# Kernel tuning notes

Measured on AMD Instinct MI355X. Metric: run time of the kernel, lower is better.

The kernel has to match this reference:

```python
import jax, jax.numpy as jnp
import numpy as np

NUM_GROUPS = 8
NUM_HEADS = 4
EPS = 1e-5


def group_norm(x, w, b):
    # x: [B, C, H, W]; normalize over (C/G, H, W) within each of G groups
    B, C, H, W = x.shape
    xg = x.reshape(B, NUM_GROUPS, C // NUM_GROUPS, H, W)
    mean = xg.mean(axis=(2, 3, 4), keepdims=True)
    var = xg.var(axis=(2, 3, 4), keepdims=True)
    xn = ((xg - mean) * jax.lax.rsqrt(var + EPS)).reshape(B, C, H, W)
    return xn * w[None, :, None, None] + b[None, :, None, None]


def setup_inputs() -> dict:
    key = jax.random.key(0)
    ks = jax.random.split(key, 7)
    B, C, H, W = 4, 256, 64, 64
    x = jax.random.normal(ks[0], (B, C, H, W), dtype=jnp.float32)
    gn_w = jax.random.normal(ks[1], (C,), dtype=jnp.float32) * 0.1 + 1.0
    gn_b = jax.random.normal(ks[2], (C,), dtype=jnp.float32) * 0.1
    qkv_w = jax.random.normal(ks[3], (3 * C, C), dtype=jnp.float32) / np.sqrt(C)
    qkv_b = jax.random.normal(ks[4], (3 * C,), dtype=jnp.float32) * 0.02
    proj_w = jax.random.normal(ks[5], (C, C), dtype=jnp.float32) / np.sqrt(C)
    proj_b = jax.random.normal(ks[6], (C,), dtype=jnp.float32) * 0.02
    return {"x": x, "gn_w": gn_w, "gn_b": gn_b, "qkv_w": qkv_w,
            "qkv_b": qkv_b, "proj_w": proj_w, "proj_b": proj_b}


def reference(x, gn_w, gn_b, qkv_w, qkv_b, proj_w, proj_b):
    B, C, H, W = x.shape
    nh = NUM_HEADS
    hd = C // nh
    scale = hd ** -0.5
    N = H * W

    h = group_norm(x, gn_w, gn_b)
    # 1x1 conv == channel matmul: [B, 3C, H, W]
    qkv = jnp.einsum('oc,bchw->bohw', qkv_w, h) + qkv_b[None, :, None, None]
    qkv = qkv.reshape(B, 3, nh, hd, N)  # matches torch .view(B,3,nh,hd,HW)
    q, k, v = qkv[:, 0], qkv[:, 1], qkv[:, 2]  # each [B, nh, hd, N]

    attn = jnp.einsum('bhdn,bhdm->bhnm', q, k) * scale  # [B, nh, N, N]
    attn = jax.nn.softmax(attn, axis=-1)
    out = jnp.einsum('bhnm,bhdm->bhdn', attn, v)  # [B, nh, hd, N]
    out = out.reshape(B, C, H, W)

    proj = jnp.einsum('oc,bchw->bohw', proj_w, out) + proj_b[None, :, None, None]
    return x + proj
```

## Files before the change

kernel.cpp:

```cpp
#include <hip/hip_runtime.h>
#include <hip/hip_bf16.h>

#define BB   4
#define CC   256
#define NN   4096
#define NH   4
#define HD   64
#define NG   8
#define GSZ  32
#define EPSV 1e-5f
#define SCALE_L2E 0.18033688f

typedef __bf16 bf16x8 __attribute__((ext_vector_type(8)));
typedef float  f32x4  __attribute__((ext_vector_type(4)));
typedef short  short4v __attribute__((ext_vector_type(4)));

#define MFMA16(a, b, c)  __builtin_amdgcn_mfma_f32_16x16x32_bf16((a), (b), (c), 0, 0, 0)
#define MFMAPV(a, b, c)  __builtin_amdgcn_mfma_f32_16x16x16bf16_1k((a), (b), (c), 0, 0, 0)

#if __has_builtin(__builtin_amdgcn_exp2f)
#define EXP2F __builtin_amdgcn_exp2f
#else
#define EXP2F exp2f
#endif

__device__ inline unsigned short f2bf(float f) {
    unsigned int u = __float_as_uint(f);
    u += 0x7fffu + ((u >> 16) & 1u);
    return (unsigned short)(u >> 16);
}

__device__ __forceinline__ short4v pk4(const f32x4& p) {
    alignas(8) unsigned int u[2];
    u[0] = __builtin_amdgcn_perm(__float_as_uint(p[1]), __float_as_uint(p[0]), 0x07060302u);
    u[1] = __builtin_amdgcn_perm(__float_as_uint(p[3]), __float_as_uint(p[2]), 0x07060302u);
    return *reinterpret_cast<short4v*>(u);
}

__device__ __forceinline__ void async_ld16(void* lds, const void* g) {
    __builtin_amdgcn_global_load_lds(
        (const __attribute__((address_space(1))) unsigned int*)g,
        (__attribute__((address_space(3))) unsigned int*)lds, 16, 0, 0);
}

__global__ void k_prep(const float* __restrict__ x, float* __restrict__ stats,
                       const float* __restrict__ wq, const float* __restrict__ wp,
                       unsigned short* __restrict__ oq, unsigned short* __restrict__ op) {
    int blk = blockIdx.x;
    int t = threadIdx.x;
    if (blk >= 256) {
        int i = (blk - 256) * 256 + t;
        if (i < 3 * CC * CC) oq[i] = f2bf(wq[i]);
        if (i < CC * CC)     op[i] = f2bf(wp[i]);
        return;
    }
    int b = blk >> 6, g = (blk >> 3) & 7, s = blk & 7;
    const float* p = x + ((size_t)(b * CC + g * GSZ)) * NN + s * 16384;
    float s0 = 0.f, s1 = 0.f;
    #pragma unroll
    for (int i = 0; i < 64; ++i) { float v = p[i * 256 + t]; s0 += v; s1 += v * v; }
    #pragma unroll
    for (int m = 1; m <= 32; m <<= 1) { s0 += __shfl_xor(s0, m); s1 += __shfl_xor(s1, m); }
    __shared__ float ls[8];
    int w = t >> 6;
    if ((t & 63) == 0) { ls[w * 2] = s0; ls[w * 2 + 1] = s1; }
    __syncthreads();
    if (t == 0) {
        float a0 = ls[0] + ls[2] + ls[4] + ls[6];
        float a1 = ls[1] + ls[3] + ls[5] + ls[7];
        atomicAdd(&stats[(b * NG + g) * 2 + 0], a0);
        atomicAdd(&stats[(b * NG + g) * 2 + 1], a1);
    }
}

__global__ void k_gnapply(const float* __restrict__ x, const float* __restrict__ gw,
                          const float* __restrict__ gb, const float* __restrict__ stats,
                          unsigned short* __restrict__ ht) {
    int b = blockIdx.z, ct = blockIdx.y, nt = blockIdx.x;
    int c0 = ct * 32, n0 = nt * 64;
    int t = threadIdx.x;
    __shared__ float tile[32][65];
    const float* xp = x + ((size_t)(b * CC + c0)) * NN + n0;
    int cl = t >> 6, nl = t & 63;
    #pragma unroll
    for (int p = 0; p < 8; ++p)
        tile[p * 4 + cl][nl] = xp[(size_t)(p * 4 + cl) * NN + nl];
    float sum = stats[(b * NG + ct) * 2 + 0];
    float ssq = stats[(b * NG + ct) * 2 + 1];
    float mean = sum * (1.0f / 131072.0f);
    float var  = ssq * (1.0f / 131072.0f) - mean * mean;
    float inv  = rsqrtf(var + EPSV);
    __syncthreads();
    int nw = t >> 2, ci = (t & 3) * 8;
    alignas(16) unsigned short o8[8];
    #pragma unroll
    for (int j = 0; j < 8; ++j) {
        int c = c0 + ci + j;
        float v = (tile[ci + j][nw] - mean) * inv * gw[c] + gb[c];
        o8[j] = f2bf(v);
    }
    *reinterpret_cast<uint4*>(ht + ((size_t)(b * NN + n0 + nw)) * CC + c0 + ci) =
        *reinterpret_cast<const uint4*>(o8);
}

__global__ void __launch_bounds__(256)
k_qkv(const unsigned short* __restrict__ ht, const unsigned short* __restrict__ wq,
      const float* __restrict__ qb,
      unsigned short* __restrict__ qt, unsigned short* __restrict__ kt,
      unsigned short* __restrict__ vt) {
    int bx = blockIdx.x, by = blockIdx.y;
    int t = threadIdx.x, wave = t >> 6, lane = t & 63;
    int l15 = lane & 15, quad = lane >> 4;
    int wm = wave >> 1, wn = wave & 1;

    __shared__ alignas(16) unsigned char At[2][8192];
    __shared__ alignas(16) unsigned char Bt[2][8192];

    const char* Ag = (const char*)wq + (size_t)by * 65536;
    const char* Bg = (const char*)ht + (size_t)bx * 65536;
    int row0 = t >> 2, slot = t & 3;
    size_t a0 = (size_t)row0 * 512 + slot * 16;
    size_t a1 = a0 + 64 * 512;
    unsigned int dst0 = wave * 1024;

    auto stage = [&](int buf, int kk) {
        size_t ko = (size_t)kk * 64;
        async_ld16(At[buf] + dst0,        Ag + a0 + ko);
        async_ld16(At[buf] + 4096 + dst0, Ag + a1 + ko);
        async_ld16(Bt[buf] + dst0,        Bg + a0 + ko);
        async_ld16(Bt[buf] + 4096 + dst0, Bg + a1 + ko);
    };

    f32x4 acc[4][4];
    #pragma unroll
    for (int i = 0; i < 4; ++i)
        #pragma unroll
        for (int j = 0; j < 4; ++j) acc[i][j] = (f32x4){0.f, 0.f, 0.f, 0.f};

    stage(0, 0);
    __syncthreads();

    for (int kk = 0; kk < 8; ++kk) {
        int cur = kk & 1;
        if (kk < 7) stage(cur ^ 1, kk + 1);
        bf16x8 af[4], bf[4];
        #pragma unroll
        for (int f = 0; f < 4; ++f) {
            af[f] = *reinterpret_cast<const bf16x8*>(At[cur] + (wm * 64 + f * 16 + l15) * 64 + quad * 16);
            bf[f] = *reinterpret_cast<const bf16x8*>(Bt[cur] + (wn * 64 + f * 16 + l15) * 64 + quad * 16);
        }
        #pragma unroll
        for (int fm = 0; fm < 4; ++fm)
            #pragma unroll
            for (int fn = 0; fn < 4; ++fn)
                acc[fm][fn] = MFMA16(af[fm], bf[fn], acc[fm][fn]);
        __syncthreads();
    }

    int s = by >> 1;
    int nn0 = bx * 128;
    int b = nn0 >> 12, nbase = nn0 & 4095;
    #pragma unroll
    for (int fm = 0; fm < 4; ++fm) {
        int o = by * 128 + wm * 64 + fm * 16 + quad * 4;
        int h = (o >> 6) & 3, d0 = o & 63;
        float bias[4];
        #pragma unroll
        for (int r = 0; r < 4; ++r) bias[r] = qb[o + r];
        #pragma unroll
        for (int fn = 0; fn < 4; ++fn) {
            int n = nbase + wn * 64 + fn * 16 + l15;
            if (s == 0) {
                alignas(8) unsigned short o4[4];
                #pragma unroll
                for (int r = 0; r < 4; ++r) o4[r] = f2bf((acc[fm][fn][r] + bias[r]) * SCALE_L2E);
                *reinterpret_cast<uint2*>(qt + (((size_t)(b * NH + h) * NN) + n) * HD + d0) =
                    *reinterpret_cast<const uint2*>(o4);
            } else if (s == 1) {
                alignas(8) unsigned short o4[4];
                #pragma unroll
                for (int r = 0; r < 4; ++r) o4[r] = f2bf(acc[fm][fn][r] + bias[r]);
                *reinterpret_cast<uint2*>(kt + (((size_t)(b * NH + h) * NN) + n) * HD + d0) =
                    *reinterpret_cast<const uint2*>(o4);
            } else {
                #pragma unroll
                for (int r = 0; r < 4; ++r)
                    vt[((size_t)(b * NH + h) * HD + d0 + r) * NN + n] = f2bf(acc[fm][fn][r] + bias[r]);
            }
        }
    }
}

__global__ void __launch_bounds__(256)
k_attn(const unsigned short* __restrict__ qt, const unsigned short* __restrict__ kt,
       const unsigned short* __restrict__ vt,
       unsigned short* __restrict__ op0, unsigned short* __restrict__ op1,
       float* __restrict__ lip) {
    int bh = blockIdx.y;
    int split = blockIdx.z;
    int t = threadIdx.x, wave = t >> 6, lane = t & 63;
    int l15 = lane & 15, quad = lane >> 4;
    int qbase = blockIdx.x * 128 + wave * 32;
    int kbase = split * 2048;
    const unsigned short* qp = qt + (size_t)bh * NN * HD;
    const unsigned short* kp = kt + (size_t)bh * NN * HD;
    const unsigned short* vp = vt + (size_t)bh * HD * NN;

    __shared__ alignas(16) unsigned char kbuf[2][8192];
    __shared__ alignas(16) unsigned char vbuf[2][8192];

    int lr8 = lane >> 3, lc8 = lane & 7;
    int swz = lc8 ^ lr8;
    const char* ksrc = (const char*)kp + (size_t)(kbase + wave * 16 + lr8) * 128 + swz * 16;
    const char* vsrc = (const char*)vp + (size_t)(wave * 16 + lr8) * 8192 + (size_t)kbase * 2 + swz * 16;
    unsigned int dstw = wave * 2048;

    auto stage = [&](int buf) {
        async_ld16(kbuf[buf] + dstw,        ksrc);
        async_ld16(kbuf[buf] + dstw + 1024, ksrc + 1024);
        ksrc += 8192;
        async_ld16(vbuf[buf] + dstw,        vsrc);
        async_ld16(vbuf[buf] + dstw + 1024, vsrc + 8 * 8192);
        vsrc += 128;
    };

    bf16x8 qaA0 = *reinterpret_cast<const bf16x8*>(qp + (size_t)(qbase + l15) * HD + quad * 8);
    bf16x8 qaA1 = *reinterpret_cast<const bf16x8*>(qp + (size_t)(qbase + l15) * HD + 32 + quad * 8);
    bf16x8 qaB0 = *reinterpret_cast<const bf16x8*>(qp + (size_t)(qbase + 16 + l15) * HD + quad * 8);
    bf16x8 qaB1 = *reinterpret_cast<const bf16x8*>(qp + (size_t)(qbase + 16 + l15) * HD + 32 + quad * 8);

    f32x4 OA[4], OB[4];
    #pragma unroll
    for (int i = 0; i < 4; ++i) { OA[i] = (f32x4){0.f, 0.f, 0.f, 0.f}; OB[i] = (f32x4){0.f, 0.f, 0.f, 0.f}; }
    float liA = 0.f, liB = 0.f;

    int sx = l15 & 7;

    auto compute = [&](const unsigned char* kb, const unsigned char* vbb) {
        f32x4 sA0[2], sA1[2], sB0[2], sB1[2];
        #pragma unroll
        for (int s = 0; s < 2; ++s) {
            int r0 = (s * 32 + l15) * 128;
            bf16x8 k00 = *reinterpret_cast<const bf16x8*>(kb + r0 + ((quad ^ sx) * 16));
            bf16x8 k01 = *reinterpret_cast<const bf16x8*>(kb + r0 + (((quad + 4) ^ sx) * 16));
            bf16x8 k10 = *reinterpret_cast<const bf16x8*>(kb + r0 + 2048 + ((quad ^ sx) * 16));
            bf16x8 k11 = *reinterpret_cast<const bf16x8*>(kb + r0 + 2048 + (((quad + 4) ^ sx) * 16));
            sA0[s] = (f32x4){0.f,0.f,0.f,0.f};  sA1[s] = (f32x4){0.f,0.f,0.f,0.f};
            sB0[s] = (f32x4){0.f,0.f,0.f,0.f};  sB1[s] = (f32x4){0.f,0.f,0.f,0.f};
            sA0[s] = MFMA16(k00, qaA0, sA0[s]);  sA0[s] = MFMA16(k01, qaA1, sA0[s]);
            sA1[s] = MFMA16(k10, qaA0, sA1[s]);  sA1[s] = MFMA16(k11, qaA1, sA1[s]);
            sB0[s] = MFMA16(k00, qaB0, sB0[s]);  sB0[s] = MFMA16(k01, qaB1, sB0[s]);
            sB1[s] = MFMA16(k10, qaB0, sB1[s]);  sB1[s] = MFMA16(k11, qaB1, sB1[s]);
        }
        #pragma unroll
        for (int s = 0; s < 2; ++s) {
            f32x4 pA0, pA1, pB0, pB1;
            #pragma unroll
            for (int r = 0; r < 4; ++r) {
                pA0[r] = EXP2F(sA0[s][r]);  pA1[r] = EXP2F(sA1[s][r]);
                pB0[r] = EXP2F(sB0[s][r]);  pB1[r] = EXP2F(sB1[s][r]);
            }
            liA += (pA0[0] + pA0[1] + pA0[2] + pA0[3]) + (pA1[0] + pA1[1] + pA1[2] + pA1[3]);
            liB += (pB0[0] + pB0[1] + pB0[2] + pB0[3]) + (pB1[0] + pB1[1] + pB1[2] + pB1[3]);

            short4v fA0 = pk4(pA0), fA1 = pk4(pA1), fB0 = pk4(pB0), fB1 = pk4(pB1);

            #pragma unroll
            for (int dc = 0; dc < 4; ++dc) {
                int c0 = ((s * 4 + (quad >> 1)) ^ sx) * 16 + (quad & 1) * 8;
                int c1 = ((s * 4 + 2 + (quad >> 1)) ^ sx) * 16 + (quad & 1) * 8;
                const unsigned char* vrow = vbb + (dc * 16 + l15) * 128;
                short4v v0 = *reinterpret_cast<const short4v*>(vrow + c0);
                short4v v1 = *reinterpret_cast<const short4v*>(vrow + c1);
                OA[dc] = MFMAPV(fA0, v0, OA[dc]);
                OA[dc] = MFMAPV(fA1, v1, OA[dc]);
                OB[dc] = MFMAPV(fB0, v0, OB[dc]);
                OB[dc] = MFMAPV(fB1, v1, OB[dc]);
            }
        }
    };

    stage(0);
    __syncthreads();

    for (int p = 0; p < 16; ++p) {
        stage(1);
        compute(kbuf[0], vbuf[0]);
        __syncthreads();
        if (p < 15) stage(0);
        compute(kbuf[1], vbuf[1]);
        __syncthreads();
    }

    liA += __shfl_xor(liA, 16);  liA += __shfl_xor(liA, 32);
    liB += __shfl_xor(liB, 16);  liB += __shfl_xor(liB, 32);

    unsigned short* op = split ? op1 : op0;
    int b = bh >> 2, h = bh & 3;
    #pragma unroll
    for (int dc = 0; dc < 4; ++dc) {
        #pragma unroll
        for (int r = 0; r < 4; ++r) {
            int qA = qbase + quad * 4 + r;
            op[((size_t)(b * NN) + qA) * CC + h * HD + dc * 16 + l15]      = f2bf(OA[dc][r]);
            op[((size_t)(b * NN) + qA + 16) * CC + h * HD + dc * 16 + l15] = f2bf(OB[dc][r]);
        }
    }
    float* lp = lip + (size_t)split * (16 * NN) + (size_t)bh * NN + qbase;
    if (quad == 0)      lp[l15]      = liA;
    else if (quad == 1) lp[16 + l15] = liB;
}

__global__ void __launch_bounds__(256)
k_comb(unsigned short* ao, const unsigned short* __restrict__ p1, const float* __restrict__ lip) {
    int g = blockIdx.x * 256 + threadIdx.x;
    int d8 = g & 7;
    int h  = (g >> 3) & 3;
    int n  = (g >> 5) & 4095;
    int b  = g >> 17;
    int bh = b * 4 + h;
    float li0 = lip[(size_t)bh * NN + n];
    float li1 = lip[(size_t)16 * NN + (size_t)bh * NN + n];
    float inv = 1.0f / (li0 + li1);
    size_t idx = ((size_t)(b * NN) + n) * CC + h * HD + d8 * 8;
    uint4 u0 = *reinterpret_cast<const uint4*>(ao + idx);
    uint4 u1 = *reinterpret_cast<const uint4*>(p1 + idx);
    const unsigned short* a0 = reinterpret_cast<const unsigned short*>(&u0);
    const unsigned short* a1 = reinterpret_cast<const unsigned short*>(&u1);
    alignas(16) unsigned short o8[8];
    #pragma unroll
    for (int i = 0; i < 8; ++i) {
        float f0 = __uint_as_float((unsigned)a0[i] << 16);
        float f1 = __uint_as_float((unsigned)a1[i] << 16);
        o8[i] = f2bf((f0 + f1) * inv);
    }
    *reinterpret_cast<uint4*>(ao + idx) = *reinterpret_cast<const uint4*>(o8);
}

__global__ void __launch_bounds__(256)
k_proj(const unsigned short* __restrict__ ao, const unsigned short* __restrict__ wp,
       const float* __restrict__ pb, const float* __restrict__ x,
       float* __restrict__ out) {
    int bx = blockIdx.x, by = blockIdx.y;
    int t = threadIdx.x, wave = t >> 6, lane = t & 63;
    int l15 = lane & 15, quad = lane >> 4;
    int wm = wave >> 1, wn = wave & 1;

    __shared__ alignas(16) unsigned char At[2][4096];
    __shared__ alignas(16) unsigned char Bt[2][4096];

    const char* Ag = (const char*)wp + (size_t)by * 32768;
    const char* Bg = (const char*)ao + (size_t)bx * 32768;
    int row0 = t >> 2, slot = t & 3;
    size_t a0 = (size_t)row0 * 512 + slot * 16;
    unsigned int dst0 = wave * 1024;

    auto stage = [&](int buf, int kk) {
        size_t ko = (size_t)kk * 64;
        async_ld16(At[buf] + dst0, Ag + a0 + ko);
        async_ld16(Bt[buf] + dst0, Bg + a0 + ko);
    };

    f32x4 acc[2][2];
    #pragma unroll
    for (int i = 0; i < 2; ++i)
        #pragma unroll
        for (int j = 0; j < 2; ++j) acc[i][j] = (f32x4){0.f, 0.f, 0.f, 0.f};

    stage(0, 0);
    __syncthreads();

    for (int kk = 0; kk < 8; ++kk) {
        int cur = kk & 1;
        if (kk < 7) stage(cur ^ 1, kk + 1);
        bf16x8 af[2], bf[2];
        #pragma unroll
        for (int f = 0; f < 2; ++f) {
            af[f] = *reinterpret_cast<const bf16x8*>(At[cur] + (wm * 32 + f * 16 + l15) * 64 + quad * 16);
            bf[f] = *reinterpret_cast<const bf16x8*>(Bt[cur] + (wn * 32 + f * 16 + l15) * 64 + quad * 16);
        }
        #pragma unroll
        for (int fm = 0; fm < 2; ++fm)
            #pragma unroll
            for (int fn = 0; fn < 2; ++fn)
                acc[fm][fn] = MFMA16(af[fm], bf[fn], acc[fm][fn]);
        __syncthreads();
    }

    int nn0 = bx * 64;
    int b = nn0 >> 12, nbase = nn0 & 4095;
    #pragma unroll
    for (int fm = 0; fm < 2; ++fm) {
        int o = by * 64 + wm * 32 + fm * 16 + quad * 4;
        float bias[4];
        #pragma unroll
        for (int r = 0; r < 4; ++r) bias[r] = pb[o + r];
        #pragma unroll
        for (int fn = 0; fn < 2; ++fn) {
            int n = nbase + wn * 32 + fn * 16 + l15;
            #pragma unroll
            for (int r = 0; r < 4; ++r) {
                size_t idx = ((size_t)(b * CC + o + r)) * NN + n;
                out[idx] = acc[fm][fn][r] + bias[r] + x[idx];
            }
        }
    }
}

extern "C" void kernel_launch(void* const* d_in, const int* in_sizes, int n_in,
                              void* d_out, int out_size, void* d_ws, size_t ws_size,
                              hipStream_t stream) {
    const float* x     = (const float*)d_in[0];
    const float* gw    = (const float*)d_in[1];
    const float* gb    = (const float*)d_in[2];
    const float* qkvw  = (const float*)d_in[3];
    const float* qkvb  = (const float*)d_in[4];
    const float* projw = (const float*)d_in[5];
    const float* projb = (const float*)d_in[6];
    float* out = (float*)d_out;

    char* w = (char*)d_ws;
    size_t off = 0;
    unsigned short* ht = (unsigned short*)(w + off); off += (size_t)BB * NN * CC * 2;
    unsigned short* qt = (unsigned short*)(w + off); off += (size_t)BB * NH * NN * HD * 2;
    unsigned short* kt = (unsigned short*)(w + off); off += (size_t)BB * NH * NN * HD * 2;
    unsigned short* vt = (unsigned short*)(w + off); off += (size_t)BB * NH * HD * NN * 2;
    unsigned short* ao = (unsigned short*)(w + off); off += (size_t)BB * NN * CC * 2;
    unsigned short* wqb = (unsigned short*)(w + off); off += (size_t)3 * CC * CC * 2;
    unsigned short* wpb = (unsigned short*)(w + off); off += (size_t)CC * CC * 2;
    float* stats = (float*)(w + off); off += BB * NG * 2 * sizeof(float);
    float* lip   = (float*)(w + off); off += (size_t)2 * 16 * NN * sizeof(float);

    hipMemsetAsync(stats, 0, BB * NG * 2 * sizeof(float), stream);
    k_prep<<<1024, 256, 0, stream>>>(x, stats, qkvw, projw, wqb, wpb);
    k_gnapply<<<dim3(NN / 64, CC / 32, BB), 256, 0, stream>>>(x, gw, gb, stats, ht);
    k_qkv<<<dim3(BB * NN / 128, 6), 256, 0, stream>>>(ht, wqb, qkvb, qt, kt, vt);
    k_attn<<<dim3(NN / 128, BB * NH, 2), 256, 0, stream>>>(qt, kt, vt, ao, ht, lip);
    k_comb<<<2048, 256, 0, stream>>>(ao, ht, lip);
    k_proj<<<dim3(BB * NN / 64, CC / 64), 256, 0, stream>>>(ao, wpb, projb, x, out);
}
```

Baseline: 214.6 us.

## Use 16x16x32 MFMA for PV by permuting V layout in QKV store

The V tensor columns are stored in a permuted order within each 32-token block, so each lane's eight probability values line up with one contiguous 16-byte V load. This lets the P·V product use the K=32 bf16 MFMA, halving the MFMA count and the LDS reads for V. The launch bounds also add a minimum-blocks hint of 4, which may limit registers and cause spills.

Result: faster. 191.7 us (-10.6%).

```diff
diff --git a/kernel.cpp b/kernel.cpp
--- a/kernel.cpp
+++ b/kernel.cpp
@@ -13,10 +13,8 @@
 
 typedef __bf16 bf16x8 __attribute__((ext_vector_type(8)));
 typedef float  f32x4  __attribute__((ext_vector_type(4)));
-typedef short  short4v __attribute__((ext_vector_type(4)));
 
 #define MFMA16(a, b, c)  __builtin_amdgcn_mfma_f32_16x16x32_bf16((a), (b), (c), 0, 0, 0)
-#define MFMAPV(a, b, c)  __builtin_amdgcn_mfma_f32_16x16x16bf16_1k((a), (b), (c), 0, 0, 0)
 
 #if __has_builtin(__builtin_amdgcn_exp2f)
 #define EXP2F __builtin_amdgcn_exp2f
@@ -30,11 +28,13 @@
     return (unsigned short)(u >> 16);
 }
 
-__device__ __forceinline__ short4v pk4(const f32x4& p) {
-    alignas(8) unsigned int u[2];
-    u[0] = __builtin_amdgcn_perm(__float_as_uint(p[1]), __float_as_uint(p[0]), 0x07060302u);
-    u[1] = __builtin_amdgcn_perm(__float_as_uint(p[3]), __float_as_uint(p[2]), 0x07060302u);
-    return *reinterpret_cast<short4v*>(u);
+__device__ __forceinline__ bf16x8 pk8(const f32x4& p0, const f32x4& p1) {
+    alignas(16) unsigned int u[4];
+    u[0] = __builtin_amdgcn_perm(__float_as_uint(p0[1]), __float_as_uint(p0[0]), 0x07060302u);
+    u[1] = __builtin_amdgcn_perm(__float_as_uint(p0[3]), __float_as_uint(p0[2]), 0x07060302u);
+    u[2] = __builtin_amdgcn_perm(__float_as_uint(p1[1]), __float_as_uint(p1[0]), 0x07060302u);
+    u[3] = __builtin_amdgcn_perm(__float_as_uint(p1[3]), __float_as_uint(p1[2]), 0x07060302u);
+    return *reinterpret_cast<bf16x8*>(u);
 }
 
 __device__ __forceinline__ void async_ld16(void* lds, const void* g) {
@@ -183,15 +183,17 @@
                 *reinterpret_cast<uint2*>(kt + (((size_t)(b * NH + h) * NN) + n) * HD + d0) =
                     *reinterpret_cast<const uint2*>(o4);
             } else {
+                int cl = n & 31;
+                int pn = (n & ~31) | (((cl & 12) << 1) | ((cl >> 4) << 2) | (cl & 3));
                 #pragma unroll
                 for (int r = 0; r < 4; ++r)
-                    vt[((size_t)(b * NH + h) * HD + d0 + r) * NN + n] = f2bf(acc[fm][fn][r] + bias[r]);
+                    vt[((size_t)(b * NH + h) * HD + d0 + r) * NN + pn] = f2bf(acc[fm][fn][r] + bias[r]);
             }
         }
     }
 }
 
-__global__ void __launch_bounds__(256)
+__global__ void __launch_bounds__(256, 4)
 k_attn(const unsigned short* __restrict__ qt, const unsigned short* __restrict__ kt,
        const unsigned short* __restrict__ vt,
        unsigned short* __restrict__ op0, unsigned short* __restrict__ op1,
@@ -263,19 +265,15 @@
             liA += (pA0[0] + pA0[1] + pA0[2] + pA0[3]) + (pA1[0] + pA1[1] + pA1[2] + pA1[3]);
             liB += (pB0[0] + pB0[1] + pB0[2] + pB0[3]) + (pB1[0] + pB1[1] + pB1[2] + pB1[3]);
 
-            short4v fA0 = pk4(pA0), fA1 = pk4(pA1), fB0 = pk4(pB0), fB1 = pk4(pB1);
+            bf16x8 fA = pk8(pA0, pA1);
+            bf16x8 fB = pk8(pB0, pB1);
 
             #pragma unroll
             for (int dc = 0; dc < 4; ++dc) {
-                int c0 = ((s * 4 + (quad >> 1)) ^ sx) * 16 + (quad & 1) * 8;
-                int c1 = ((s * 4 + 2 + (quad >> 1)) ^ sx) * 16 + (quad & 1) * 8;
                 const unsigned char* vrow = vbb + (dc * 16 + l15) * 128;
-                short4v v0 = *reinterpret_cast<const short4v*>(vrow + c0);
-                short4v v1 = *reinterpret_cast<const short4v*>(vrow + c1);
-                OA[dc] = MFMAPV(fA0, v0, OA[dc]);
-                OA[dc] = MFMAPV(fA1, v1, OA[dc]);
-                OB[dc] = MFMAPV(fB0, v0, OB[dc]);
-                OB[dc] = MFMAPV(fB1, v1, OB[dc]);
+                bf16x8 vv = *reinterpret_cast<const bf16x8*>(vrow + (((s * 4 + quad) ^ sx) * 16));
+                OA[dc] = MFMA16(fA, vv, OA[dc]);
+                OB[dc] = MFMA16(fB, vv, OB[dc]);
             }
         }
     };
```
